# Performance work log

Measured on AMD Instinct MI355X. Metric: run time of the kernel, lower is better.

The kernel has to match this reference:

```python
import jax, jax.numpy as jnp
import numpy as np

N_ENTITY = 100000
H_DIM = 512
N_ROWS = 262144
ALPHA = 0.5          # EMA rate for fast state
GATE_TH = 0.5        # gate_threshold buffer
GATE_SCALE = 5.0     # gate_scale buffer
LN_EPS = 1e-5


def setup_inputs() -> dict:
    key = jax.random.key(0)
    k1, k2, k3, k4, k5 = jax.random.split(key, 5)
    entity_emb = jax.random.normal(k1, (N_ROWS, H_DIM), dtype=jnp.float32)
    entity_ids = jax.random.randint(k2, (N_ROWS,), 0, N_ENTITY, dtype=jnp.int64)
    slow_state = 0.1 * jax.random.normal(k3, (N_ENTITY, H_DIM), dtype=jnp.float32)
    fast_state = 0.1 * jax.random.normal(k4, (N_ENTITY, H_DIM), dtype=jnp.float32)
    # torch nn.Linear(2h, h): weight shape (h, 2h), y = x @ W.T + b
    W = jax.random.normal(k5, (H_DIM, 2 * H_DIM), dtype=jnp.float32) * 0.02
    b = jnp.zeros((H_DIM,), dtype=jnp.float32)
    return {"entity_emb": entity_emb, "slow_state": slow_state,
            "fast_state": fast_state, "W": W, "b": b, "entity_ids": entity_ids}


def _layer_norm(x):
    mu = jnp.mean(x, axis=-1, keepdims=True)
    var = jnp.mean(jnp.square(x - mu), axis=-1, keepdims=True)
    return (x - mu) * jax.lax.rsqrt(var + LN_EPS)


def reference(entity_emb, slow_state, fast_state, W, b, entity_ids):
    # ---- fuse_with_state (gate path) ----
    state = slow_state[entity_ids]                                   # (N, h) gather
    is_active = (jnp.sum(jnp.abs(state), axis=-1, keepdims=True) > 1e-6).astype(entity_emb.dtype)
    h_state = _layer_norm(state)
    gate_in = jnp.concatenate([entity_emb, h_state], axis=-1)        # (N, 2h)
    z = jax.nn.sigmoid(gate_in @ W.T + b)                            # (N, h)
    fused = z * entity_emb + (1.0 - z) * h_state
    out = is_active * fused + (1.0 - is_active) * entity_emb

    # ---- writeback (no-grad in torch; scatter-reduce EMA + norm-gated slow update) ----
    ctx = jax.lax.stop_gradient(out)
    ids = entity_ids
    counts = jax.ops.segment_sum(jnp.ones((ctx.shape[0],), ctx.dtype), ids,
                                 num_segments=N_ENTITY)              # (E,)
    ctx_sum = jax.ops.segment_sum(ctx, ids, num_segments=N_ENTITY)   # (E, h)
    ctx_mean = ctx_sum / jnp.clip(counts, 1.0)[:, None]
    touched = (counts > 0)[:, None]
    new_fast_all = (1.0 - ALPHA) * fast_state + ALPHA * ctx_mean
    new_fast = jnp.where(touched, new_fast_all, fast_state)
    diff = new_fast - slow_state
    delta = jnp.linalg.norm(diff, axis=-1, keepdims=True)
    gate = jax.nn.sigmoid(GATE_SCALE * (delta - GATE_TH))
    new_slow = jnp.where(touched, slow_state + gate * diff, slow_state)
    return out, new_fast, new_slow
```

## Files before the change

### kernel.cpp

```cpp
#include <hip/hip_runtime.h>
#include <hip/hip_bf16.h>
#include <cstdint>

#define NROWS 262144
#define HDIM  512
#define NENT  100000
#define SCAN_NBLK ((NENT + 1023) / 1024)

typedef __attribute__((ext_vector_type(4))) float  f32x4;
typedef __attribute__((ext_vector_type(8))) short  bf16x8;

static __device__ __forceinline__ unsigned short f2bf(float x) {
    unsigned u = __float_as_uint(x);
    u += 0x7FFF + ((u >> 16) & 1);
    return (unsigned short)(u >> 16);
}

__global__ void pack_w_kernel(const float* __restrict__ W, unsigned short* __restrict__ Wp) {
    int g    = blockIdx.x * 256 + threadIdx.x;
    int lane = g & 63;
    int task = g >> 6;
    int nt   = task >> 5;
    int kt   = task & 31;
    int col  = nt * 16 + (lane & 15);
    int k    = kt * 32 + ((lane >> 4) << 3);
    const float* src = W + (size_t)col * 1024 + k;
    f32x4 v0 = *(const f32x4*)(src);
    f32x4 v1 = *(const f32x4*)(src + 4);
    bf16x8 ov;
#pragma unroll
    for (int i = 0; i < 4; ++i) {
        ov[i]     = (short)f2bf(v0[i]);
        ov[4 + i] = (short)f2bf(v1[i]);
    }
    *(bf16x8*)(Wp + (size_t)g * 8) = ov;
}

__global__ __launch_bounds__(256) void count_kernel(const int* __restrict__ ids,
                                                    unsigned* __restrict__ counts) {
    int r = blockIdx.x * 256 + threadIdx.x;
    if (r < NROWS) atomicAdd(&counts[ids[r]], 1u);
}

__global__ __launch_bounds__(1024) void scan1_kernel(const unsigned* __restrict__ counts,
                                                     unsigned* __restrict__ off,
                                                     unsigned* __restrict__ bsums) {
    __shared__ unsigned tmp[1024];
    int i = blockIdx.x * 1024 + threadIdx.x;
    unsigned v = (i < NENT) ? counts[i] : 0u;
    tmp[threadIdx.x] = v;
    __syncthreads();
#pragma unroll
    for (int o = 1; o < 1024; o <<= 1) {
        unsigned a = (threadIdx.x >= o) ? tmp[threadIdx.x - o] : 0u;
        __syncthreads();
        tmp[threadIdx.x] += a;
        __syncthreads();
    }
    if (i < NENT) off[i] = tmp[threadIdx.x] - v;
    if (threadIdx.x == 1023) bsums[blockIdx.x] = tmp[1023];
}

__global__ void scan2_kernel(unsigned* __restrict__ bsums) {
    if (threadIdx.x == 0 && blockIdx.x == 0) {
        unsigned s = 0;
        for (int i = 0; i < SCAN_NBLK; ++i) { unsigned t = bsums[i]; bsums[i] = s; s += t; }
    }
}

__global__ __launch_bounds__(1024) void scan3_kernel(unsigned* __restrict__ off,
                                                     const unsigned* __restrict__ bsums,
                                                     unsigned* __restrict__ cursor) {
    int i = blockIdx.x * 1024 + threadIdx.x;
    if (i < NENT) {
        unsigned o = off[i] + bsums[blockIdx.x];
        off[i] = o;
        cursor[i] = o;
    }
    if (i == 0) off[NENT] = NROWS;
}

__global__ __launch_bounds__(256) void fill_kernel(const int* __restrict__ ids,
                                                   unsigned* __restrict__ cursor,
                                                   int* __restrict__ rowidx) {
    int r = blockIdx.x * 256 + threadIdx.x;
    if (r < NROWS) {
        unsigned p = atomicAdd(&cursor[ids[r]], 1u);
        rowidx[p] = r;
    }
}

__global__ __launch_bounds__(512) void fuse_kernel(
    const float* __restrict__ emb, const float* __restrict__ slow,
    const unsigned short* __restrict__ Wp, const float* __restrict__ bias,
    const int* __restrict__ ids, float* __restrict__ out)
{
    __shared__ unsigned short aLds[8 * 512];
    __shared__ float muS[64], rsS[64], actS[64], bS[512];
    __shared__ int idS[64];

    const int t    = threadIdx.x;
    const int w    = t >> 6;
    const int lane = t & 63;
    const int brow = blockIdx.x * 64;

    if (t < 128) ((f32x4*)bS)[t] = ((const f32x4*)bias)[t];

    for (int rr = 0; rr < 8; ++rr) {
        int row = w * 8 + rr;
        int id  = ids[brow + row];
        const float* sp = slow + (size_t)id * HDIM;
        f32x4 v0 = ((const f32x4*)sp)[lane * 2];
        f32x4 v1 = ((const f32x4*)sp)[lane * 2 + 1];
        float s = 0.f, s2 = 0.f, sa = 0.f;
#pragma unroll
        for (int i = 0; i < 4; ++i) {
            s  += v0[i] + v1[i];
            s2 += v0[i] * v0[i] + v1[i] * v1[i];
            sa += fabsf(v0[i]) + fabsf(v1[i]);
        }
#pragma unroll
        for (int m = 32; m >= 1; m >>= 1) {
            s  += __shfl_xor(s, m);
            s2 += __shfl_xor(s2, m);
            sa += __shfl_xor(sa, m);
        }
        if (lane == 0) {
            float mu  = s * (1.f / HDIM);
            float var = s2 * (1.f / HDIM) - mu * mu;
            muS[row]  = mu;
            rsS[row]  = rsqrtf(var + 1e-5f);
            actS[row] = (sa > 1e-6f) ? 1.f : 0.f;
            idS[row]  = id;
        }
    }
    __syncthreads();

    const int rowS = t >> 3;
    const int kc   = t & 7;
    const float* embRow = emb + (size_t)(brow + rowS) * HDIM;
    const float* stRow  = slow + (size_t)idS[rowS] * HDIM;
    const float muR = muS[rowS], rsR = rsS[rowS];

    const int rt_s = rowS >> 4, rl_s = rowS & 15;
    const int kt_s = kc >> 2,  kg_s = kc & 3;
    unsigned short* aDst = &aLds[(kt_s * 4 + rt_s) * 512 + (kg_s * 16 + (rl_s ^ (kg_s << 1))) * 8];
    const int kgr = lane >> 4, rlr = lane & 15;
    const int posr = kgr * 16 + (rlr ^ (kgr << 1));

    const int c0 = w * 64;
    f32x4 zero4 = {0.f, 0.f, 0.f, 0.f};
    f32x4 acc[4][4];
#pragma unroll
    for (int i = 0; i < 4; ++i)
#pragma unroll
        for (int j = 0; j < 4; ++j) acc[i][j] = zero4;

    for (int ks = 0; ks < 16; ++ks) {
        f32x4 x0, x1;
        int kb = ks * 64 + kc * 8;
        if (ks < 8) {
            x0 = *(const f32x4*)(embRow + kb);
            x1 = *(const f32x4*)(embRow + kb + 4);
        } else {
            x0 = *(const f32x4*)(stRow + kb - 512);
            x1 = *(const f32x4*)(stRow + kb - 512 + 4);
#pragma unroll
            for (int i = 0; i < 4; ++i) {
                x0[i] = (x0[i] - muR) * rsR;
                x1[i] = (x1[i] - muR) * rsR;
            }
        }
        __syncthreads();
        bf16x8 av;
#pragma unroll
        for (int i = 0; i < 4; ++i) {
            av[i]     = (short)f2bf(x0[i]);
            av[4 + i] = (short)f2bf(x1[i]);
        }
        *(bf16x8*)aDst = av;
        __syncthreads();

#pragma unroll
        for (int kk = 0; kk < 2; ++kk) {
            bf16x8 a0 = *(const bf16x8*)&aLds[(kk * 4 + 0) * 512 + posr * 8];
            bf16x8 a1 = *(const bf16x8*)&aLds[(kk * 4 + 1) * 512 + posr * 8];
            bf16x8 a2 = *(const bf16x8*)&aLds[(kk * 4 + 2) * 512 + posr * 8];
            bf16x8 a3 = *(const bf16x8*)&aLds[(kk * 4 + 3) * 512 + posr * 8];
            int kt32 = ks * 2 + kk;
#pragma unroll
            for (int ct = 0; ct < 4; ++ct) {
                int ntile = (c0 >> 4) + ct;
                bf16x8 bfr = *(const bf16x8*)(Wp + ((size_t)(ntile * 32 + kt32) * 64 + lane) * 8);
                acc[0][ct] = __builtin_amdgcn_mfma_f32_16x16x32_bf16(bfr, a0, acc[0][ct], 0, 0, 0);
                acc[1][ct] = __builtin_amdgcn_mfma_f32_16x16x32_bf16(bfr, a1, acc[1][ct], 0, 0, 0);
                acc[2][ct] = __builtin_amdgcn_mfma_f32_16x16x32_bf16(bfr, a2, acc[2][ct], 0, 0, 0);
                acc[3][ct] = __builtin_amdgcn_mfma_f32_16x16x32_bf16(bfr, a3, acc[3][ct], 0, 0, 0);
            }
        }
    }

#pragma unroll
    for (int rt = 0; rt < 4; ++rt) {
        int rowl = rt * 16 + (lane & 15);
        int grow = brow + rowl;
        int id   = idS[rowl];
        float mu = muS[rowl], rs = rsS[rowl], act = actS[rowl];
        const float* embP  = emb  + (size_t)grow * HDIM;
        const float* slowP = slow + (size_t)id * HDIM;
        float*       outP  = out  + (size_t)grow * HDIM;
#pragma unroll
        for (int ct = 0; ct < 4; ++ct) {
            int col0 = c0 + ct * 16 + ((lane >> 4) << 2);
            f32x4 bv = *(const f32x4*)&bS[col0];
            f32x4 ev = *(const f32x4*)(embP + col0);
            f32x4 sv = *(const f32x4*)(slowP + col0);
            f32x4 o;
#pragma unroll
            for (int r = 0; r < 4; ++r) {
                float logit = acc[rt][ct][r] + bv[r];
                float z  = 1.f / (1.f + __expf(-logit));
                float h  = (sv[r] - mu) * rs;
                float fused = z * ev[r] + (1.f - z) * h;
                o[r] = (act > 0.f) ? fused : ev[r];
            }
            *(f32x4*)(outP + col0) = o;
        }
    }
}

__global__ __launch_bounds__(256) void finalize_kernel(
    const float* __restrict__ fast, const float* __restrict__ slow,
    const float* __restrict__ out, const unsigned* __restrict__ off,
    const int* __restrict__ rowidx, float* __restrict__ nf, float* __restrict__ ns)
{
    int e = blockIdx.x * 4 + (threadIdx.x >> 6);
    if (e >= NENT) return;
    int lane = threadIdx.x & 63;
    size_t base = (size_t)e * HDIM + lane * 8;

    f32x4 f0 = *(const f32x4*)(fast + base), f1 = *(const f32x4*)(fast + base + 4);
    f32x4 l0 = *(const f32x4*)(slow + base), l1 = *(const f32x4*)(slow + base + 4);

    unsigned o0 = off[e], o1 = off[e + 1];
    int c = (int)(o1 - o0);

    if (c == 0) {
        *(f32x4*)(nf + base)     = f0;
        *(f32x4*)(nf + base + 4) = f1;
        *(f32x4*)(ns + base)     = l0;
        *(f32x4*)(ns + base + 4) = l1;
        return;
    }

    f32x4 s0 = {0.f, 0.f, 0.f, 0.f}, s1 = {0.f, 0.f, 0.f, 0.f};
    for (int j = 0; j < c; ++j) {
        int r = rowidx[o0 + j];
        const float* p = out + (size_t)r * HDIM + lane * 8;
        s0 += *(const f32x4*)p;
        s1 += *(const f32x4*)(p + 4);
    }

    float inv = 0.5f / (float)c;
    f32x4 n0, n1, d0, d1;
    float ss = 0.f;
#pragma unroll
    for (int i = 0; i < 4; ++i) {
        n0[i] = 0.5f * f0[i] + s0[i] * inv;
        n1[i] = 0.5f * f1[i] + s1[i] * inv;
        d0[i] = n0[i] - l0[i]; ss += d0[i] * d0[i];
        d1[i] = n1[i] - l1[i]; ss += d1[i] * d1[i];
    }
#pragma unroll
    for (int m = 32; m >= 1; m >>= 1) ss += __shfl_xor(ss, m);
    float delta = sqrtf(ss);
    float gate  = 1.f / (1.f + expf(-5.f * (delta - 0.5f)));

    f32x4 o0v, o1v;
#pragma unroll
    for (int i = 0; i < 4; ++i) {
        o0v[i] = l0[i] + gate * d0[i];
        o1v[i] = l1[i] + gate * d1[i];
    }
    *(f32x4*)(nf + base)     = n0;
    *(f32x4*)(nf + base + 4) = n1;
    *(f32x4*)(ns + base)     = o0v;
    *(f32x4*)(ns + base + 4) = o1v;
}

extern "C" void kernel_launch(void* const* d_in, const int* in_sizes, int n_in,
                              void* d_out, int out_size, void* d_ws, size_t ws_size,
                              hipStream_t stream) {
    const float* emb  = (const float*)d_in[0];
    const float* slow = (const float*)d_in[1];
    const float* fast = (const float*)d_in[2];
    const float* W    = (const float*)d_in[3];
    const float* bias = (const float*)d_in[4];
    const int*   ids  = (const int*)d_in[5];

    float* out = (float*)d_out;
    float* nf  = out + (size_t)NROWS * HDIM;
    float* ns  = nf + (size_t)NENT * HDIM;

    unsigned short* Wp   = (unsigned short*)d_ws;
    unsigned* counts     = (unsigned*)((char*)d_ws + (1u << 20));
    unsigned* off        = (unsigned*)((char*)d_ws + (1u << 20) + 512 * 1024);
    unsigned* bsums      = (unsigned*)((char*)d_ws + (2u << 20));
    int*      rowidx     = (int*)((char*)d_ws + (2u << 20) + 4096);

    hipMemsetAsync(counts, 0, (size_t)NENT * sizeof(unsigned), stream);

    pack_w_kernel<<<256, 256, 0, stream>>>(W, Wp);
    count_kernel<<<NROWS / 256, 256, 0, stream>>>(ids, counts);
    scan1_kernel<<<SCAN_NBLK, 1024, 0, stream>>>(counts, off, bsums);
    scan2_kernel<<<1, 64, 0, stream>>>(bsums);
    scan3_kernel<<<SCAN_NBLK, 1024, 0, stream>>>(off, bsums, counts);
    fill_kernel<<<NROWS / 256, 256, 0, stream>>>(ids, counts, rowidx);
    fuse_kernel<<<NROWS / 64, 512, 0, stream>>>(emb, slow, Wp, bias, ids, out);
    finalize_kernel<<<(NENT + 3) / 4, 256, 0, stream>>>(fast, slow, out, off, rowidx, nf, ns);
}
```

Baseline: 985.3 us.

## Double-buffer A tile in LDS and prefetch next K-slice during MFMA

The A operand staging buffer in LDS becomes a pair of buffers. The global loads for step ks+1 are issued before the MFMA work of step ks, and the packed bf16 data goes into the other buffer afterwards. This drops one of the two barriers per K step and hides global load latency behind compute. It also adds launch_bounds min-blocks 4, which caps registers and may cause spills in exchange for occupancy.

```diff
diff --git a/kernel.cpp b/kernel.cpp
--- a/kernel.cpp
+++ b/kernel.cpp
@@ -90,12 +90,12 @@
     }
 }
 
-__global__ __launch_bounds__(512) void fuse_kernel(
+__global__ __launch_bounds__(512, 4) void fuse_kernel(
     const float* __restrict__ emb, const float* __restrict__ slow,
     const unsigned short* __restrict__ Wp, const float* __restrict__ bias,
     const int* __restrict__ ids, float* __restrict__ out)
 {
-    __shared__ unsigned short aLds[8 * 512];
+    __shared__ unsigned short aLds[2][8 * 512];
     __shared__ float muS[64], rsS[64], actS[64], bS[512];
     __shared__ int idS[64];
 
@@ -144,7 +144,7 @@
 
     const int rt_s = rowS >> 4, rl_s = rowS & 15;
     const int kt_s = kc >> 2,  kg_s = kc & 3;
-    unsigned short* aDst = &aLds[(kt_s * 4 + rt_s) * 512 + (kg_s * 16 + (rl_s ^ (kg_s << 1))) * 8];
+    const int aOff = (kt_s * 4 + rt_s) * 512 + (kg_s * 16 + (rl_s ^ (kg_s << 1))) * 8;
     const int kgr = lane >> 4, rlr = lane & 15;
     const int posr = kgr * 16 + (rlr ^ (kgr << 1));
 
@@ -156,37 +156,52 @@
 #pragma unroll
         for (int j = 0; j < 4; ++j) acc[i][j] = zero4;
 
+#define LOAD_X(ks, x0, x1)                                            \
+    {   int kb = (ks) * 64 + kc * 8;                                  \
+        if ((ks) < 8) {                                               \
+            x0 = *(const f32x4*)(embRow + kb);                        \
+            x1 = *(const f32x4*)(embRow + kb + 4);                    \
+        } else {                                                      \
+            x0 = *(const f32x4*)(stRow + kb - 512);                   \
+            x1 = *(const f32x4*)(stRow + kb - 512 + 4);               \
+        }                                                             \
+    }
+
+#define PACK_STORE(ks, x0, x1, buf)                                   \
+    {   f32x4 y0 = x0, y1 = x1;                                       \
+        if ((ks) >= 8) {                                              \
+            _Pragma("unroll")                                         \
+            for (int i = 0; i < 4; ++i) {                             \
+                y0[i] = (y0[i] - muR) * rsR;                          \
+                y1[i] = (y1[i] - muR) * rsR;                          \
+            }                                                         \
+        }                                                             \
+        bf16x8 av;                                                    \
+        _Pragma("unroll")                                             \
+        for (int i = 0; i < 4; ++i) {                                 \
+            av[i]     = (short)f2bf(y0[i]);                           \
+            av[4 + i] = (short)f2bf(y1[i]);                           \
+        }                                                             \
+        *(bf16x8*)&aLds[buf][aOff] = av;                              \
+    }
+
+    {   f32x4 p0, p1;
+        LOAD_X(0, p0, p1);
+        PACK_STORE(0, p0, p1, 0);
+    }
+    __syncthreads();
+
     for (int ks = 0; ks < 16; ++ks) {
-        f32x4 x0, x1;
-        int kb = ks * 64 + kc * 8;
-        if (ks < 8) {
-            x0 = *(const f32x4*)(embRow + kb);
-            x1 = *(const f32x4*)(embRow + kb + 4);
-        } else {
-            x0 = *(const f32x4*)(stRow + kb - 512);
-            x1 = *(const f32x4*)(stRow + kb - 512 + 4);
-#pragma unroll
-            for (int i = 0; i < 4; ++i) {
-                x0[i] = (x0[i] - muR) * rsR;
-                x1[i] = (x1[i] - muR) * rsR;
-            }
-        }
-        __syncthreads();
-        bf16x8 av;
-#pragma unroll
-        for (int i = 0; i < 4; ++i) {
-            av[i]     = (short)f2bf(x0[i]);
-            av[4 + i] = (short)f2bf(x1[i]);
-        }
-        *(bf16x8*)aDst = av;
-        __syncthreads();
+        const int cur = ks & 1;
+        f32x4 n0, n1;
+        if (ks < 15) LOAD_X(ks + 1, n0, n1);
 
 #pragma unroll
         for (int kk = 0; kk < 2; ++kk) {
-            bf16x8 a0 = *(const bf16x8*)&aLds[(kk * 4 + 0) * 512 + posr * 8];
-            bf16x8 a1 = *(const bf16x8*)&aLds[(kk * 4 + 1) * 512 + posr * 8];
-            bf16x8 a2 = *(const bf16x8*)&aLds[(kk * 4 + 2) * 512 + posr * 8];
-            bf16x8 a3 = *(const bf16x8*)&aLds[(kk * 4 + 3) * 512 + posr * 8];
+            bf16x8 a0 = *(const bf16x8*)&aLds[cur][(kk * 4 + 0) * 512 + posr * 8];
+            bf16x8 a1 = *(const bf16x8*)&aLds[cur][(kk * 4 + 1) * 512 + posr * 8];
+            bf16x8 a2 = *(const bf16x8*)&aLds[cur][(kk * 4 + 2) * 512 + posr * 8];
+            bf16x8 a3 = *(const bf16x8*)&aLds[cur][(kk * 4 + 3) * 512 + posr * 8];
             int kt32 = ks * 2 + kk;
 #pragma unroll
             for (int ct = 0; ct < 4; ++ct) {
@@ -198,7 +213,12 @@
                 acc[3][ct] = __builtin_amdgcn_mfma_f32_16x16x32_bf16(bfr, a3, acc[3][ct], 0, 0, 0);
             }
         }
-    }
+
+        if (ks < 15) PACK_STORE(ks + 1, n0, n1, cur ^ 1);
+        __syncthreads();
+    }
+#undef LOAD_X
+#undef PACK_STORE
 
 #pragma unroll
     for (int rt = 0; rt < 4; ++rt) {
```

Result: slower. 1.043 ms (+5.9%).

## Double-buffer A tiles in fuse kernel with 1024-thread blocks and prefetched W fragments

Applied to the files above, without the earlier changes.

Restructures the fused gate GEMM to use 16 waves per 64-row block, each owning 32 output columns. The A tile is double-buffered in LDS in 128-wide K phases, state columns first, so the next phase's global load and bf16 pack overlap the current phase's MFMAs. This drops one barrier per step and preloads W fragments into registers. The goal is to hide global-load latency and barrier stalls, at the cost of more LDS and more threads per block, which may limit occupancy.

```diff
diff --git a/kernel.cpp b/kernel.cpp
--- a/kernel.cpp
+++ b/kernel.cpp
@@ -90,12 +90,12 @@
     }
 }
 
-__global__ __launch_bounds__(512) void fuse_kernel(
+__global__ __launch_bounds__(1024) void fuse_kernel(
     const float* __restrict__ emb, const float* __restrict__ slow,
     const unsigned short* __restrict__ Wp, const float* __restrict__ bias,
     const int* __restrict__ ids, float* __restrict__ out)
 {
-    __shared__ unsigned short aLds[8 * 512];
+    __shared__ unsigned short aLds[2][16 * 512];
     __shared__ float muS[64], rsS[64], actS[64], bS[512];
     __shared__ int idS[64];
 
@@ -106,8 +106,8 @@
 
     if (t < 128) ((f32x4*)bS)[t] = ((const f32x4*)bias)[t];
 
-    for (int rr = 0; rr < 8; ++rr) {
-        int row = w * 8 + rr;
+    for (int rr = 0; rr < 4; ++rr) {
+        int row = w * 4 + rr;
         int id  = ids[brow + row];
         const float* sp = slow + (size_t)id * HDIM;
         f32x4 v0 = ((const f32x4*)sp)[lane * 2];
@@ -136,70 +136,93 @@
     }
     __syncthreads();
 
-    const int rowS = t >> 3;
-    const int kc   = t & 7;
+    const int rowS = t >> 4;
+    const int c    = t & 15;
     const float* embRow = emb + (size_t)(brow + rowS) * HDIM;
     const float* stRow  = slow + (size_t)idS[rowS] * HDIM;
     const float muR = muS[rowS], rsR = rsS[rowS];
 
-    const int rt_s = rowS >> 4, rl_s = rowS & 15;
-    const int kt_s = kc >> 2,  kg_s = kc & 3;
-    unsigned short* aDst = &aLds[(kt_s * 4 + rt_s) * 512 + (kg_s * 16 + (rl_s ^ (kg_s << 1))) * 8];
+    const int kg_s = c & 3;
+    const int aOff = ((c >> 2) * 4 + (rowS >> 4)) * 512 +
+                     (kg_s * 16 + ((rowS & 15) ^ (kg_s << 1))) * 8;
     const int kgr = lane >> 4, rlr = lane & 15;
     const int posr = kgr * 16 + (rlr ^ (kgr << 1));
 
-    const int c0 = w * 64;
     f32x4 zero4 = {0.f, 0.f, 0.f, 0.f};
-    f32x4 acc[4][4];
+    f32x4 acc[4][2];
 #pragma unroll
     for (int i = 0; i < 4; ++i)
 #pragma unroll
-        for (int j = 0; j < 4; ++j) acc[i][j] = zero4;
-
-    for (int ks = 0; ks < 16; ++ks) {
-        f32x4 x0, x1;
-        int kb = ks * 64 + kc * 8;
-        if (ks < 8) {
-            x0 = *(const f32x4*)(embRow + kb);
-            x1 = *(const f32x4*)(embRow + kb + 4);
-        } else {
-            x0 = *(const f32x4*)(stRow + kb - 512);
-            x1 = *(const f32x4*)(stRow + kb - 512 + 4);
-#pragma unroll
-            for (int i = 0; i < 4; ++i) {
-                x0[i] = (x0[i] - muR) * rsR;
-                x1[i] = (x1[i] - muR) * rsR;
+        for (int j = 0; j < 2; ++j) acc[i][j] = zero4;
+
+#define LOAD_X(ph, x0, x1)                                              \
+    {   const float* base = ((ph) < 4) ? (stRow + (ph) * 128 + c * 8)   \
+                                       : (embRow + ((ph) - 4) * 128 + c * 8); \
+        x0 = *(const f32x4*)(base);                                     \
+        x1 = *(const f32x4*)(base + 4);                                 \
+    }
+
+#define PACK_STORE(ph, x0, x1, buf)                                     \
+    {   f32x4 y0 = x0, y1 = x1;                                         \
+        if ((ph) < 4) {                                                 \
+            _Pragma("unroll")                                           \
+            for (int i = 0; i < 4; ++i) {                               \
+                y0[i] = (y0[i] - muR) * rsR;                            \
+                y1[i] = (y1[i] - muR) * rsR;                            \
+            }                                                           \
+        }                                                               \
+        bf16x8 av;                                                      \
+        _Pragma("unroll")                                               \
+        for (int i = 0; i < 4; ++i) {                                   \
+            av[i]     = (short)f2bf(y0[i]);                             \
+            av[4 + i] = (short)f2bf(y1[i]);                             \
+        }                                                               \
+        *(bf16x8*)&aLds[buf][aOff] = av;                                \
+    }
+
+    {   f32x4 p0, p1;
+        LOAD_X(0, p0, p1);
+        PACK_STORE(0, p0, p1, 0);
+    }
+    __syncthreads();
+
+    for (int ph = 0; ph < 8; ++ph) {
+        const int cur = ph & 1;
+        const int ktW = (ph < 4) ? (16 + ph * 4) : ((ph - 4) * 4);
+
+        bf16x8 wf[8];
+#pragma unroll
+        for (int kk = 0; kk < 4; ++kk)
+#pragma unroll
+            for (int ct = 0; ct < 2; ++ct)
+                wf[kk * 2 + ct] = *(const bf16x8*)(
+                    Wp + ((size_t)((w * 2 + ct) * 32 + ktW + kk) * 64 + lane) * 8);
+
+        f32x4 nx0, nx1;
+        if (ph < 7) LOAD_X(ph + 1, nx0, nx1);
+
+#pragma unroll
+        for (int kk = 0; kk < 4; ++kk) {
+            bf16x8 a0 = *(const bf16x8*)&aLds[cur][(kk * 4 + 0) * 512 + posr * 8];
+            bf16x8 a1 = *(const bf16x8*)&aLds[cur][(kk * 4 + 1) * 512 + posr * 8];
+            bf16x8 a2 = *(const bf16x8*)&aLds[cur][(kk * 4 + 2) * 512 + posr * 8];
+            bf16x8 a3 = *(const bf16x8*)&aLds[cur][(kk * 4 + 3) * 512 + posr * 8];
+#pragma unroll
+            for (int ct = 0; ct < 2; ++ct) {
+                acc[0][ct] = __builtin_amdgcn_mfma_f32_16x16x32_bf16(wf[kk * 2 + ct], a0, acc[0][ct], 0, 0, 0);
+                acc[1][ct] = __builtin_amdgcn_mfma_f32_16x16x32_bf16(wf[kk * 2 + ct], a1, acc[1][ct], 0, 0, 0);
+                acc[2][ct] = __builtin_amdgcn_mfma_f32_16x16x32_bf16(wf[kk * 2 + ct], a2, acc[2][ct], 0, 0, 0);
+                acc[3][ct] = __builtin_amdgcn_mfma_f32_16x16x32_bf16(wf[kk * 2 + ct], a3, acc[3][ct], 0, 0, 0);
             }
         }
+
+        if (ph < 7) PACK_STORE(ph + 1, nx0, nx1, cur ^ 1);
         __syncthreads();
-        bf16x8 av;
-#pragma unroll
-        for (int i = 0; i < 4; ++i) {
-            av[i]     = (short)f2bf(x0[i]);
-            av[4 + i] = (short)f2bf(x1[i]);
-        }
-        *(bf16x8*)aDst = av;
-        __syncthreads();
-
-#pragma unroll
-        for (int kk = 0; kk < 2; ++kk) {
-            bf16x8 a0 = *(const bf16x8*)&aLds[(kk * 4 + 0) * 512 + posr * 8];
-            bf16x8 a1 = *(const bf16x8*)&aLds[(kk * 4 + 1) * 512 + posr * 8];
-            bf16x8 a2 = *(const bf16x8*)&aLds[(kk * 4 + 2) * 512 + posr * 8];
-            bf16x8 a3 = *(const bf16x8*)&aLds[(kk * 4 + 3) * 512 + posr * 8];
-            int kt32 = ks * 2 + kk;
-#pragma unroll
-            for (int ct = 0; ct < 4; ++ct) {
-                int ntile = (c0 >> 4) + ct;
-                bf16x8 bfr = *(const bf16x8*)(Wp + ((size_t)(ntile * 32 + kt32) * 64 + lane) * 8);
-                acc[0][ct] = __builtin_amdgcn_mfma_f32_16x16x32_bf16(bfr, a0, acc[0][ct], 0, 0, 0);
-                acc[1][ct] = __builtin_amdgcn_mfma_f32_16x16x32_bf16(bfr, a1, acc[1][ct], 0, 0, 0);
-                acc[2][ct] = __builtin_amdgcn_mfma_f32_16x16x32_bf16(bfr, a2, acc[2][ct], 0, 0, 0);
-                acc[3][ct] = __builtin_amdgcn_mfma_f32_16x16x32_bf16(bfr, a3, acc[3][ct], 0, 0, 0);
-            }
-        }
-    }
-
+    }
+#undef LOAD_X
+#undef PACK_STORE
+
+    const int c0 = w * 32;
 #pragma unroll
     for (int rt = 0; rt < 4; ++rt) {
         int rowl = rt * 16 + (lane & 15);
@@ -210,7 +233,7 @@
         const float* slowP = slow + (size_t)id * HDIM;
         float*       outP  = out  + (size_t)grow * HDIM;
 #pragma unroll
-        for (int ct = 0; ct < 4; ++ct) {
+        for (int ct = 0; ct < 2; ++ct) {
             int col0 = c0 + ct * 16 + ((lane >> 4) << 2);
             f32x4 bv = *(const f32x4*)&bS[col0];
             f32x4 ev = *(const f32x4*)(embP + col0);
@@ -316,6 +339,6 @@
     scan2_kernel<<<1, 64, 0, stream>>>(bsums);
     scan3_kernel<<<SCAN_NBLK, 1024, 0, stream>>>(off, bsums, counts);
     fill_kernel<<<NROWS / 256, 256, 0, stream>>>(ids, counts, rowidx);
-    fuse_kernel<<<NROWS / 64, 512, 0, stream>>>(emb, slow, Wp, bias, ids, out);
+    fuse_kernel<<<NROWS / 64, 1024, 0, stream>>>(emb, slow, Wp, bias, ids, out);
     finalize_kernel<<<(NENT + 3) / 4, 256, 0, stream>>>(fast, slow, out, off, rowidx, nf, ns);
 }
```

Result: no change. 979.7 us (-0.6%).

## Stage full bf16 activation tile in LDS, halve rows per block, double-buffer loads

Applied to the files above, without the earlier changes.

The fuse kernel now loads all 32 rows by 1024 K of activations (embedding plus normalized slow state) into LDS as bf16 once, instead of streaming 64-wide K slices with two barriers each. The MFMA loop then runs without barriers and double-buffers the weight and activation fragments in registers. The epilogue reads emb and normalized state from the bf16 LDS copy instead of re-reading fp32 from global memory. Block tiles shrink to 32 rows, giving twice as many blocks. In exchange, the output is computed from bf16-rounded emb and h values, which costs precision, and each weight fragment is reused across fewer rows.

```diff
diff --git a/kernel.cpp b/kernel.cpp
--- a/kernel.cpp
+++ b/kernel.cpp
@@ -14,6 +14,10 @@
     unsigned u = __float_as_uint(x);
     u += 0x7FFF + ((u >> 16) & 1);
     return (unsigned short)(u >> 16);
+}
+static __device__ __forceinline__ float bf2f(unsigned short h) {
+    unsigned u = ((unsigned)h) << 16;
+    return __uint_as_float(u);
 }
 
 __global__ void pack_w_kernel(const float* __restrict__ W, unsigned short* __restrict__ Wp) {
@@ -90,24 +94,24 @@
     }
 }
 
-__global__ __launch_bounds__(512) void fuse_kernel(
+__global__ __launch_bounds__(512, 4) void fuse_kernel(
     const float* __restrict__ emb, const float* __restrict__ slow,
     const unsigned short* __restrict__ Wp, const float* __restrict__ bias,
     const int* __restrict__ ids, float* __restrict__ out)
 {
-    __shared__ unsigned short aLds[8 * 512];
-    __shared__ float muS[64], rsS[64], actS[64], bS[512];
-    __shared__ int idS[64];
+    __shared__ unsigned short xLds[64 * 64 * 8];
+    __shared__ float muS[32], rsS[32], actS[32], bS[512];
+    __shared__ int idS[32];
 
     const int t    = threadIdx.x;
     const int w    = t >> 6;
     const int lane = t & 63;
-    const int brow = blockIdx.x * 64;
+    const int brow = blockIdx.x * 32;
 
     if (t < 128) ((f32x4*)bS)[t] = ((const f32x4*)bias)[t];
 
-    for (int rr = 0; rr < 8; ++rr) {
-        int row = w * 8 + rr;
+    for (int rr = 0; rr < 4; ++rr) {
+        int row = w * 4 + rr;
         int id  = ids[brow + row];
         const float* sp = slow + (size_t)id * HDIM;
         f32x4 v0 = ((const f32x4*)sp)[lane * 2];
@@ -136,93 +140,102 @@
     }
     __syncthreads();
 
-    const int rowS = t >> 3;
-    const int kc   = t & 7;
-    const float* embRow = emb + (size_t)(brow + rowS) * HDIM;
-    const float* stRow  = slow + (size_t)idS[rowS] * HDIM;
-    const float muR = muS[rowS], rsR = rsS[rowS];
-
-    const int rt_s = rowS >> 4, rl_s = rowS & 15;
-    const int kt_s = kc >> 2,  kg_s = kc & 3;
-    unsigned short* aDst = &aLds[(kt_s * 4 + rt_s) * 512 + (kg_s * 16 + (rl_s ^ (kg_s << 1))) * 8];
-    const int kgr = lane >> 4, rlr = lane & 15;
-    const int posr = kgr * 16 + (rlr ^ (kgr << 1));
-
-    const int c0 = w * 64;
-    f32x4 zero4 = {0.f, 0.f, 0.f, 0.f};
-    f32x4 acc[4][4];
-#pragma unroll
-    for (int i = 0; i < 4; ++i)
-#pragma unroll
-        for (int j = 0; j < 4; ++j) acc[i][j] = zero4;
-
-    for (int ks = 0; ks < 16; ++ks) {
+    for (int slot = t; slot < 4096; slot += 512) {
+        int T    = slot >> 6;
+        int ls   = slot & 63;
+        int kt   = T >> 1;
+        int row  = (T & 1) * 16 + (ls & 15);
+        int k    = kt * 32 + ((ls >> 4) << 3);
         f32x4 x0, x1;
-        int kb = ks * 64 + kc * 8;
-        if (ks < 8) {
-            x0 = *(const f32x4*)(embRow + kb);
-            x1 = *(const f32x4*)(embRow + kb + 4);
+        if (k < 512) {
+            const float* p = emb + (size_t)(brow + row) * HDIM + k;
+            x0 = *(const f32x4*)p;
+            x1 = *(const f32x4*)(p + 4);
         } else {
-            x0 = *(const f32x4*)(stRow + kb - 512);
-            x1 = *(const f32x4*)(stRow + kb - 512 + 4);
+            const float* p = slow + (size_t)idS[row] * HDIM + (k - 512);
+            x0 = *(const f32x4*)p;
+            x1 = *(const f32x4*)(p + 4);
+            float mu = muS[row], rs = rsS[row];
 #pragma unroll
             for (int i = 0; i < 4; ++i) {
-                x0[i] = (x0[i] - muR) * rsR;
-                x1[i] = (x1[i] - muR) * rsR;
+                x0[i] = (x0[i] - mu) * rs;
+                x1[i] = (x1[i] - mu) * rs;
             }
         }
-        __syncthreads();
         bf16x8 av;
 #pragma unroll
         for (int i = 0; i < 4; ++i) {
             av[i]     = (short)f2bf(x0[i]);
             av[4 + i] = (short)f2bf(x1[i]);
         }
-        *(bf16x8*)aDst = av;
-        __syncthreads();
-
-#pragma unroll
-        for (int kk = 0; kk < 2; ++kk) {
-            bf16x8 a0 = *(const bf16x8*)&aLds[(kk * 4 + 0) * 512 + posr * 8];
-            bf16x8 a1 = *(const bf16x8*)&aLds[(kk * 4 + 1) * 512 + posr * 8];
-            bf16x8 a2 = *(const bf16x8*)&aLds[(kk * 4 + 2) * 512 + posr * 8];
-            bf16x8 a3 = *(const bf16x8*)&aLds[(kk * 4 + 3) * 512 + posr * 8];
-            int kt32 = ks * 2 + kk;
-#pragma unroll
-            for (int ct = 0; ct < 4; ++ct) {
-                int ntile = (c0 >> 4) + ct;
-                bf16x8 bfr = *(const bf16x8*)(Wp + ((size_t)(ntile * 32 + kt32) * 64 + lane) * 8);
-                acc[0][ct] = __builtin_amdgcn_mfma_f32_16x16x32_bf16(bfr, a0, acc[0][ct], 0, 0, 0);
-                acc[1][ct] = __builtin_amdgcn_mfma_f32_16x16x32_bf16(bfr, a1, acc[1][ct], 0, 0, 0);
-                acc[2][ct] = __builtin_amdgcn_mfma_f32_16x16x32_bf16(bfr, a2, acc[2][ct], 0, 0, 0);
-                acc[3][ct] = __builtin_amdgcn_mfma_f32_16x16x32_bf16(bfr, a3, acc[3][ct], 0, 0, 0);
-            }
-        }
-    }
-
-#pragma unroll
-    for (int rt = 0; rt < 4; ++rt) {
+        ((bf16x8*)xLds)[slot] = av;
+    }
+    __syncthreads();
+
+    f32x4 zero4 = {0.f, 0.f, 0.f, 0.f};
+    f32x4 acc[2][4];
+#pragma unroll
+    for (int i = 0; i < 2; ++i)
+#pragma unroll
+        for (int j = 0; j < 4; ++j) acc[i][j] = zero4;
+
+    const unsigned short* wpL = Wp + (size_t)lane * 8;
+
+#define LOADW(dst, kt)                                                  \
+    _Pragma("unroll")                                                   \
+    for (int ct = 0; ct < 4; ++ct)                                      \
+        dst[ct] = *(const bf16x8*)(wpL + ((size_t)((w * 4 + ct) * 32 + (kt)) << 9));
+
+#define LOADX(dst, kt)                                                  \
+    _Pragma("unroll")                                                   \
+    for (int rt = 0; rt < 2; ++rt)                                      \
+        dst[rt] = ((const bf16x8*)xLds)[((kt) * 2 + rt) * 64 + lane];
+
+#define MFMA_STEP(wf, xf)                                               \
+    _Pragma("unroll")                                                   \
+    for (int ct = 0; ct < 4; ++ct) {                                    \
+        acc[0][ct] = __builtin_amdgcn_mfma_f32_16x16x32_bf16(wf[ct], xf[0], acc[0][ct], 0, 0, 0); \
+        acc[1][ct] = __builtin_amdgcn_mfma_f32_16x16x32_bf16(wf[ct], xf[1], acc[1][ct], 0, 0, 0); \
+    }
+
+    bf16x8 wA[4], wB[4], xA[2], xB[2];
+    LOADW(wA, 0);
+    LOADX(xA, 0);
+    for (int kt = 0; kt < 32; kt += 2) {
+        if (kt + 1 < 32) { LOADW(wB, kt + 1); LOADX(xB, kt + 1); }
+        MFMA_STEP(wA, xA);
+        if (kt + 2 < 32) { LOADW(wA, kt + 2); LOADX(xA, kt + 2); }
+        if (kt + 1 < 32) MFMA_STEP(wB, xB);
+    }
+#undef LOADW
+#undef LOADX
+#undef MFMA_STEP
+
+#pragma unroll
+    for (int rt = 0; rt < 2; ++rt) {
         int rowl = rt * 16 + (lane & 15);
         int grow = brow + rowl;
-        int id   = idS[rowl];
         float mu = muS[rowl], rs = rsS[rowl], act = actS[rowl];
-        const float* embP  = emb  + (size_t)grow * HDIM;
-        const float* slowP = slow + (size_t)id * HDIM;
-        float*       outP  = out  + (size_t)grow * HDIM;
+        (void)mu; (void)rs;
+        float* outP = out + (size_t)grow * HDIM;
 #pragma unroll
         for (int ct = 0; ct < 4; ++ct) {
-            int col0 = c0 + ct * 16 + ((lane >> 4) << 2);
+            int col0 = w * 64 + ct * 16 + ((lane >> 4) << 2);
+            int Te = ((col0 >> 5) * 2 + rt) * 64 + (((col0 >> 3) & 3) << 4) + (lane & 15);
+            const unsigned short* pe = xLds + Te * 8 + (col0 & 7);
+            int kh = 512 + col0;
+            int Th = ((kh >> 5) * 2 + rt) * 64 + (((kh >> 3) & 3) << 4) + (lane & 15);
+            const unsigned short* ph = xLds + Th * 8 + (kh & 7);
             f32x4 bv = *(const f32x4*)&bS[col0];
-            f32x4 ev = *(const f32x4*)(embP + col0);
-            f32x4 sv = *(const f32x4*)(slowP + col0);
             f32x4 o;
 #pragma unroll
             for (int r = 0; r < 4; ++r) {
+                float ev = bf2f(pe[r]);
+                float hv = bf2f(ph[r]);
                 float logit = acc[rt][ct][r] + bv[r];
                 float z  = 1.f / (1.f + __expf(-logit));
-                float h  = (sv[r] - mu) * rs;
-                float fused = z * ev[r] + (1.f - z) * h;
-                o[r] = (act > 0.f) ? fused : ev[r];
+                float fused = z * ev + (1.f - z) * hv;
+                o[r] = (act > 0.f) ? fused : ev;
             }
             *(f32x4*)(outP + col0) = o;
         }
@@ -316,6 +329,6 @@
     scan2_kernel<<<1, 64, 0, stream>>>(bsums);
     scan3_kernel<<<SCAN_NBLK, 1024, 0, stream>>>(off, bsums, counts);
     fill_kernel<<<NROWS / 256, 256, 0, stream>>>(ids, counts, rowidx);
-    fuse_kernel<<<NROWS / 64, 512, 0, stream>>>(emb, slow, Wp, bias, ids, out);
+    fuse_kernel<<<NROWS / 32, 512, 0, stream>>>(emb, slow, Wp, bias, ids, out);
     finalize_kernel<<<(NENT + 3) / 4, 256, 0, stream>>>(fast, slow, out, off, rowidx, nf, ns);
 }
```

New measurement: 941.8 us. -4.4%, faster.
